# Kernel tuning notes

Measured on AMD Instinct MI355X. Metric: run time of the kernel, lower is better.

The kernel has to match this reference:

```python
import jax, jax.numpy as jnp
import numpy as np

C = 256
NUM_HEADS = 8
GROUPS = 8
EPS = 1e-5


def setup_inputs() -> dict:
    key = jax.random.key(0)
    ks = jax.random.split(key, 7)
    B, H, W = 2, 64, 64
    x = jax.random.normal(ks[0], (B, C, H, W), dtype=jnp.float32)
    gn_weight = jnp.ones((C,), dtype=jnp.float32)
    gn_bias = jnp.zeros((C,), dtype=jnp.float32)
    # 1x1 convs == per-pixel linear layers
    w_qkv = jax.random.normal(ks[1], (3 * C, C), dtype=jnp.float32) * (1.0 / np.sqrt(C))
    b_qkv = jax.random.normal(ks[2], (3 * C,), dtype=jnp.float32) * 0.01
    w_proj = jax.random.normal(ks[3], (C, C), dtype=jnp.float32) * (1.0 / np.sqrt(C))
    b_proj = jax.random.normal(ks[4], (C,), dtype=jnp.float32) * 0.01
    return {"x": x, "gn_weight": gn_weight, "gn_bias": gn_bias,
            "w_qkv": w_qkv, "b_qkv": b_qkv, "w_proj": w_proj, "b_proj": b_proj}


def reference(x, gn_weight, gn_bias, w_qkv, b_qkv, w_proj, b_proj):
    B, Cc, H, W = x.shape
    nh = NUM_HEADS
    hd = Cc // nh
    N = H * W
    scale = hd ** (-0.5)

    # GroupNorm(8, C): normalize over (C/G, H, W) per group, biased variance
    xg = x.reshape(B, GROUPS, Cc // GROUPS, H, W)
    mean = xg.mean(axis=(2, 3, 4), keepdims=True)
    var = xg.var(axis=(2, 3, 4), keepdims=True)
    hn = (xg - mean) * jax.lax.rsqrt(var + EPS)
    hn = hn.reshape(B, Cc, H, W) * gn_weight[None, :, None, None] + gn_bias[None, :, None, None]

    hf = hn.reshape(B, Cc, N)                       # [B, C, N]
    qkv = jnp.einsum('oc,bcn->bon', w_qkv, hf) + b_qkv[None, :, None]  # [B, 3C, N]
    qkv = qkv.reshape(B, 3, nh, hd, N)
    # q,k,v: [B, nh, N, hd]
    q = jnp.transpose(qkv[:, 0], (0, 1, 3, 2))
    k = jnp.transpose(qkv[:, 1], (0, 1, 3, 2))
    v = jnp.transpose(qkv[:, 2], (0, 1, 3, 2))

    attn = jnp.einsum('bhqd,bhkd->bhqk', q, k) * scale  # [B, nh, N, N]
    attn = jax.nn.softmax(attn, axis=-1)
    o = jnp.einsum('bhqk,bhkd->bhqd', attn, v)           # [B, nh, N, hd]
    o = jnp.transpose(o, (0, 1, 3, 2)).reshape(B, Cc, H, W)

    of = o.reshape(B, Cc, N)
    out = jnp.einsum('oc,bcn->bon', w_proj, of) + b_proj[None, :, None]
    return out.reshape(B, Cc, H, W)
```

## Files before the change

### kernel.cpp

```cpp
#include <hip/hip_runtime.h>


typedef _Float16 half8 __attribute__((ext_vector_type(8)));
typedef __fp16   fp16x2 __attribute__((ext_vector_type(2)));
typedef float    f32x4 __attribute__((ext_vector_type(4)));
typedef int      int2v __attribute__((ext_vector_type(2)));
typedef int      int4v __attribute__((ext_vector_type(4)));

__device__ __forceinline__ f32x4 mfma16(half8 a, half8 b, f32x4 c) {
  return __builtin_amdgcn_mfma_f32_16x16x32_f16(a, b, c, 0, 0, 0);
}

#if __has_builtin(__builtin_amdgcn_exp2f)
#define EXP2(x) __builtin_amdgcn_exp2f(x)
#else
#define EXP2(x) exp2f(x)
#endif

__device__ __forceinline__ unsigned short h_bits(_Float16 h) {
  return __builtin_bit_cast(unsigned short, h);
}
__device__ __forceinline__ int h2_bits(fp16x2 h) {
  return __builtin_bit_cast(int, h);
}
__device__ __forceinline__ half8 pack8(f32x4 lo, f32x4 hi) {
  int4v u;
  u[0] = h2_bits(__builtin_amdgcn_cvt_pkrtz(lo[0], lo[1]));
  u[1] = h2_bits(__builtin_amdgcn_cvt_pkrtz(lo[2], lo[3]));
  u[2] = h2_bits(__builtin_amdgcn_cvt_pkrtz(hi[0], hi[1]));
  u[3] = h2_bits(__builtin_amdgcn_cvt_pkrtz(hi[2], hi[3]));
  return __builtin_bit_cast(half8, u);
}

constexpr float CSCALE = (float)(1.4426950408889634 / 5.656854249492381);
constexpr float VSCALE = 0.0009765625f;
constexpr float VUNSC  = 1024.0f;

__global__ __launch_bounds__(256) void gn_stats(const float* __restrict__ x,
                                                float* __restrict__ stats) {
  const int bg = blockIdx.x, ch = blockIdx.y, tid = threadIdx.x;
  const float* p = x + (size_t)bg * 131072 + (size_t)ch * 4096;
  float s = 0.f, ss = 0.f;
#pragma unroll
  for (int j = 0; j < 4; ++j) {
    f32x4 v = *(const f32x4*)(p + j * 1024 + tid * 4);
#pragma unroll
    for (int k = 0; k < 4; ++k) { s += v[k]; ss += v[k] * v[k]; }
  }
#pragma unroll
  for (int m = 1; m <= 32; m <<= 1) { s += __shfl_xor(s, m); ss += __shfl_xor(ss, m); }
  __shared__ float red[8];
  const int wv = tid >> 6;
  if ((tid & 63) == 0) { red[wv * 2] = s; red[wv * 2 + 1] = ss; }
  __syncthreads();
  if (tid == 0) {
    float S = red[0] + red[2] + red[4] + red[6];
    float SS = red[1] + red[3] + red[5] + red[7];
    atomicAdd(&stats[bg * 2], S);
    atomicAdd(&stats[bg * 2 + 1], SS);
  }
}

__global__ __launch_bounds__(256) void gn_apply(const float* __restrict__ x,
                                                const float* __restrict__ gw,
                                                const float* __restrict__ gb,
                                                const float* __restrict__ stats,
                                                _Float16* __restrict__ hn) {
  __shared__ float tile[64 * 65];
  const int tid = threadIdx.x;
  const int a = tid & 15;
  const int row16 = tid >> 4;
  const int b = blockIdx.z, c0 = blockIdx.y * 64, n0 = blockIdx.x * 64;
#pragma unroll
  for (int m = 0; m < 4; ++m) {
    const int cl = row16 + 16 * m;
    const int c = c0 + cl;
    const int g = c >> 5;
    const float s = stats[(b * 8 + g) * 2];
    const float ss = stats[(b * 8 + g) * 2 + 1];
    const float mean = s * (1.f / 131072.f);
    const float var = ss * (1.f / 131072.f) - mean * mean;
    const float rstd = rsqrtf(var + 1e-5f);
    const float ga = gw[c] * rstd;
    const float be = gb[c] - mean * ga;
    f32x4 xv = *(const f32x4*)(x + ((size_t)(b * 256 + c)) * 4096 + n0 + a * 4);
#pragma unroll
    for (int j = 0; j < 4; ++j) tile[cl * 65 + a * 4 + j] = xv[j] * ga + be;
  }
  __syncthreads();
#pragma unroll
  for (int m = 0; m < 4; ++m) {
    const int nl = row16 + 16 * m;
    const int cb = a * 4;
    int2v uh;
    unsigned short hh[4];
#pragma unroll
    for (int j = 0; j < 4; ++j) {
      hh[j] = h_bits((_Float16)tile[(cb + j) * 65 + nl]);
    }
    uh[0] = hh[0] | (hh[1] << 16); uh[1] = hh[2] | (hh[3] << 16);
    size_t off = ((size_t)(b * 4096 + n0 + nl)) * 256 + c0 + cb;
    *(int2v*)(hn + off) = uh;
  }
}

template <int MODE>
__global__ __launch_bounds__(256) void gemm_f16(
    const float* __restrict__ W, const _Float16* __restrict__ Bm,
    const float* __restrict__ bias,
    _Float16* __restrict__ qkT, _Float16* __restrict__ v_t,
    float* __restrict__ outp) {
  __shared__ _Float16 a_lds[2][4096];
  __shared__ _Float16 b_lds[2][4096];
  const int tid = threadIdx.x, lane = tid & 63, wv = tid >> 6;
  const int qq = lane >> 4, ii = lane & 15;
  const int m0 = blockIdx.x * 64, n0 = blockIdx.y * 64, bz = blockIdx.z;

  const float*    asrc[2];
  const _Float16* bsrc[2];
  int dst8[2];
#pragma unroll
  for (int rep = 0; rep < 2; ++rep) {
    const int idx = tid + 256 * rep;
    dst8[rep] = idx * 8;
    const int j = idx >> 7, c = (idx >> 6) & 1, l = idx & 63;
    const int lq = l >> 4, li = l & 15;
    asrc[rep] = W + (size_t)(m0 + 16 * j + li) * 256 + 32 * c + 8 * lq;
    bsrc[rep] = Bm + ((size_t)(bz * 4096 + n0 + 16 * j + li)) * 256 + 32 * c + 8 * lq;
  }

  f32x4 acc[4] = {};

  f32x4 a0a = *(const f32x4*)asrc[0], a0b = *(const f32x4*)(asrc[0] + 4);
  f32x4 a1a = *(const f32x4*)asrc[1], a1b = *(const f32x4*)(asrc[1] + 4);
  half8 br0 = *(const half8*)bsrc[0];
  half8 br1 = *(const half8*)bsrc[1];
  *(half8*)(a_lds[0] + dst8[0]) = pack8(a0a, a0b);
  *(half8*)(a_lds[0] + dst8[1]) = pack8(a1a, a1b);
  *(half8*)(b_lds[0] + dst8[0]) = br0;
  *(half8*)(b_lds[0] + dst8[1]) = br1;
  __syncthreads();

  for (int it = 0; it < 4; ++it) {
    const int cur = it & 1;
    if (it < 3) {
      const int ko = (it + 1) * 64;
      a0a = *(const f32x4*)(asrc[0] + ko);
      a0b = *(const f32x4*)(asrc[0] + ko + 4);
      a1a = *(const f32x4*)(asrc[1] + ko);
      a1b = *(const f32x4*)(asrc[1] + ko + 4);
      br0 = *(const half8*)(bsrc[0] + ko);
      br1 = *(const half8*)(bsrc[1] + ko);
    }
    half8 ah0 = *(const half8*)(a_lds[cur] + ((wv * 2 + 0) * 64 + lane) * 8);
    half8 ah1 = *(const half8*)(a_lds[cur] + ((wv * 2 + 1) * 64 + lane) * 8);
#pragma unroll
    for (int t = 0; t < 4; ++t) {
      half8 b0 = *(const half8*)(b_lds[cur] + ((t * 2 + 0) * 64 + lane) * 8);
      half8 b1 = *(const half8*)(b_lds[cur] + ((t * 2 + 1) * 64 + lane) * 8);
      acc[t] = mfma16(ah0, b0, acc[t]);
      acc[t] = mfma16(ah1, b1, acc[t]);
    }
    if (it < 3) {
      _Float16* an = a_lds[cur ^ 1];
      _Float16* bn = b_lds[cur ^ 1];
      *(half8*)(an + dst8[0]) = pack8(a0a, a0b);
      *(half8*)(an + dst8[1]) = pack8(a1a, a1b);
      *(half8*)(bn + dst8[0]) = br0;
      *(half8*)(bn + dst8[1]) = br1;
    }
    __syncthreads();
  }

  const int och0 = m0 + 16 * wv + 4 * qq;
  if (MODE == 0) {
    if (m0 < 512) {
      const float sc = (m0 < 256) ? CSCALE : 1.0f;
#pragma unroll
      for (int t = 0; t < 4; ++t) {
        const int n = n0 + 16 * t + ii;
        unsigned short hh[4];
#pragma unroll
        for (int r = 0; r < 4; ++r) {
          hh[r] = h_bits((_Float16)((acc[t][r] + bias[och0 + r]) * sc));
        }
        int2v u;
        u[0] = hh[0] | (hh[1] << 16);
        u[1] = hh[2] | (hh[3] << 16);
        *(int2v*)(qkT + ((size_t)(bz * 4096 + n)) * 512 + och0) = u;
      }
    } else {
#pragma unroll
      for (int t = 0; t < 4; ++t) {
#pragma unroll
        for (int r = 0; r < 4; ++r) {
          const int och = och0 + r;
          const int d = och - 512;
          const int hd_ = d & 31, head = d >> 5;
          const int n = n0 + 16 * t + ii;
          v_t[((size_t)((bz * 8 + head) * 32 + hd_)) * 4096 + n] =
              (_Float16)((acc[t][r] + bias[och]) * VSCALE);
        }
      }
    }
  } else {
#pragma unroll
    for (int t = 0; t < 4; ++t) {
#pragma unroll
      for (int r = 0; r < 4; ++r) {
        const int och = och0 + r;
        const int n = n0 + 16 * t + ii;
        outp[((size_t)(bz * 256 + och)) * 4096 + n] = acc[t][r] + bias[och];
      }
    }
  }
}

__global__ __launch_bounds__(256, 8) void attn_kernel(
    const _Float16* __restrict__ qkT, const _Float16* __restrict__ v_t,
    _Float16* __restrict__ opart, float* __restrict__ lpart) {
  __shared__ _Float16 k_lds[2][2048];
  __shared__ _Float16 v_lds[2][2048];
  const int tid = threadIdx.x, lane = tid & 63, wv = tid >> 6;
  const int qq = lane >> 4, ii = lane & 15;
  const int bh = blockIdx.y, b = bh >> 3, h = bh & 7;
  const int n0 = blockIdx.x * 128;
  const int part = blockIdx.z;
  const int key0 = part * 1024;

  const _Float16* qbase =
      qkT + ((size_t)(b * 4096 + n0 + 32 * wv + ii)) * 512 + h * 32 + 8 * qq;
  half8 qf0 = *(const half8*)qbase;
  half8 qf1 = *(const half8*)(qbase + (size_t)16 * 512);

  const int f = tid >> 6, l = tid & 63;
  const int fq = l >> 4, fi = l & 15;
  const int u0 = f >> 1, hf = f & 1;
  const int g = 32 * u0 + 4 * hf + 8 * (fi >> 2) + (fi & 3);
  const _Float16* ksrc =
      qkT + ((size_t)(b * 4096 + key0 + g)) * 512 + 256 + h * 32 + 8 * fq;
  const _Float16* vsrc =
      v_t + ((size_t)(bh * 32 + 16 * hf + fi)) * 4096 + key0 + 32 * u0 + 8 * fq;
  const int dst8 = tid * 8;

  half8 ones8;
#pragma unroll
  for (int j = 0; j < 8; ++j) ones8[j] = (_Float16)1.0f;

  f32x4 o00 = {}, o10 = {}, o01 = {}, o11 = {}, accl0 = {}, accl1 = {};

  half8 kr = *(const half8*)ksrc;
  half8 vr = *(const half8*)vsrc;
  *(half8*)(k_lds[0] + dst8) = kr;
  *(half8*)(v_lds[0] + dst8) = vr;
  __syncthreads();

  for (int kb = 0; kb < 16; ++kb) {
    const int cur = kb & 1;
    if (kb < 15) {
      kr = *(const half8*)(ksrc + (size_t)(kb + 1) * 64 * 512);
      vr = *(const half8*)(vsrc + (size_t)(kb + 1) * 64);
    }
    const _Float16* kbase = k_lds[cur];
    const _Float16* vbase = v_lds[cur];

#pragma unroll
    for (int u = 0; u < 2; ++u) {
      half8 kfa = *(const half8*)(kbase + u * 1024 + lane * 8);
      half8 kfb = *(const half8*)(kbase + u * 1024 + 512 + lane * 8);
      f32x4 z = {};
      f32x4 sa0 = mfma16(kfa, qf0, z);
      f32x4 sb0 = mfma16(kfb, qf0, z);
      f32x4 sa1 = mfma16(kfa, qf1, z);
      f32x4 sb1 = mfma16(kfb, qf1, z);
      int4v p0, p1;
      p0[0] = h2_bits(__builtin_amdgcn_cvt_pkrtz(EXP2(sa0[0]), EXP2(sa0[1])));
      p0[1] = h2_bits(__builtin_amdgcn_cvt_pkrtz(EXP2(sa0[2]), EXP2(sa0[3])));
      p0[2] = h2_bits(__builtin_amdgcn_cvt_pkrtz(EXP2(sb0[0]), EXP2(sb0[1])));
      p0[3] = h2_bits(__builtin_amdgcn_cvt_pkrtz(EXP2(sb0[2]), EXP2(sb0[3])));
      p1[0] = h2_bits(__builtin_amdgcn_cvt_pkrtz(EXP2(sa1[0]), EXP2(sa1[1])));
      p1[1] = h2_bits(__builtin_amdgcn_cvt_pkrtz(EXP2(sa1[2]), EXP2(sa1[3])));
      p1[2] = h2_bits(__builtin_amdgcn_cvt_pkrtz(EXP2(sb1[0]), EXP2(sb1[1])));
      p1[3] = h2_bits(__builtin_amdgcn_cvt_pkrtz(EXP2(sb1[2]), EXP2(sb1[3])));
      half8 pt0 = __builtin_bit_cast(half8, p0);
      half8 pt1 = __builtin_bit_cast(half8, p1);
      half8 vf0 = *(const half8*)(vbase + u * 1024 + lane * 8);
      half8 vf1 = *(const half8*)(vbase + u * 1024 + 512 + lane * 8);
      o00 = mfma16(vf0, pt0, o00);
      o10 = mfma16(vf1, pt0, o10);
      accl0 = mfma16(ones8, pt0, accl0);
      o01 = mfma16(vf0, pt1, o01);
      o11 = mfma16(vf1, pt1, o11);
      accl1 = mfma16(ones8, pt1, accl1);
    }

    if (kb < 15) {
      *(half8*)(k_lds[cur ^ 1] + dst8) = kr;
      *(half8*)(v_lds[cur ^ 1] + dst8) = vr;
    }
    __syncthreads();
  }

#pragma unroll
  for (int hfq = 0; hfq < 2; ++hfq) {
    const f32x4 oa = hfq ? o01 : o00;
    const f32x4 ob = hfq ? o11 : o10;
    const int q = n0 + 32 * wv + 16 * hfq + ii;
    _Float16* base =
        opart + ((size_t)((part * 2 + b) * 4096 + q)) * 256 + h * 32;
    unsigned short hh[4];
#pragma unroll
    for (int r = 0; r < 4; ++r) hh[r] = h_bits((_Float16)oa[r]);
    int2v ua;
    ua[0] = hh[0] | (hh[1] << 16); ua[1] = hh[2] | (hh[3] << 16);
    *(int2v*)(base + 4 * qq) = ua;
#pragma unroll
    for (int r = 0; r < 4; ++r) hh[r] = h_bits((_Float16)ob[r]);
    ua[0] = hh[0] | (hh[1] << 16); ua[1] = hh[2] | (hh[3] << 16);
    *(int2v*)(base + 16 + 4 * qq) = ua;
    if (qq == 0) {
      lpart[((size_t)((part * 2 + b) * 4096 + q)) * 8 + h] =
          hfq ? accl1[0] : accl0[0];
    }
  }
}

__global__ __launch_bounds__(256) void attn_combine(
    const _Float16* __restrict__ opart, const float* __restrict__ lpart,
    _Float16* __restrict__ o16) {
  const int c = threadIdx.x, hh = c >> 5;
#pragma unroll
  for (int k = 0; k < 4; ++k) {
    const int row = blockIdx.x * 4 + k;
    const int b = row >> 12, q = row & 4095;
    float O = 0.f, L = 0.f;
#pragma unroll
    for (int p = 0; p < 4; ++p) {
      O += (float)opart[((size_t)((p * 2 + b) * 4096 + q)) * 256 + c];
      L += lpart[((size_t)((p * 2 + b) * 4096 + q)) * 8 + hh];
    }
    o16[(size_t)row * 256 + c] = (_Float16)(O * (VUNSC / L));
  }
}

extern "C" void kernel_launch(void* const* d_in, const int* in_sizes, int n_in,
                              void* d_out, int out_size, void* d_ws, size_t ws_size,
                              hipStream_t stream) {
  const float* x     = (const float*)d_in[0];
  const float* gnw   = (const float*)d_in[1];
  const float* gnb   = (const float*)d_in[2];
  const float* wqkv  = (const float*)d_in[3];
  const float* bqkv  = (const float*)d_in[4];
  const float* wproj = (const float*)d_in[5];
  const float* bproj = (const float*)d_in[6];
  float* out = (float*)d_out;

  char* ws = (char*)d_ws;
  size_t off = 0;
  auto alloc = [&](size_t bytes) -> char* {
    char* p = ws + off;
    off += (bytes + 255) & ~(size_t)255;
    return p;
  };
  float*    stats  = (float*)alloc(128);
  _Float16* hn     = (_Float16*)alloc((size_t)2 * 4096 * 256 * 2);
  _Float16* qkT    = (_Float16*)alloc((size_t)2 * 4096 * 512 * 2);
  _Float16* v_t    = (_Float16*)alloc((size_t)16 * 32 * 4096 * 2);
  _Float16* opart  = (_Float16*)alloc((size_t)8 * 4096 * 256 * 2);
  float*    lpart  = (float*)alloc((size_t)8 * 4096 * 8 * 4);
  _Float16* o16 = hn;
  if (off > ws_size) return;

  (void)hipMemsetAsync(stats, 0, 256, stream);
  gn_stats<<<dim3(16, 32), 256, 0, stream>>>(x, stats);
  gn_apply<<<dim3(64, 4, 2), 256, 0, stream>>>(x, gnw, gnb, stats, hn);
  gemm_f16<0><<<dim3(12, 64, 2), 256, 0, stream>>>(wqkv, hn, bqkv, qkT, v_t,
                                                   nullptr);
  attn_kernel<<<dim3(32, 16, 4), 256, 0, stream>>>(qkT, v_t, opart, lpart);
  attn_combine<<<2048, 256, 0, stream>>>(opart, lpart, o16);
  gemm_f16<1><<<dim3(4, 64, 2), 256, 0, stream>>>(wproj, o16, bproj, nullptr,
                                                  nullptr, out);
}
```

Measured before the change: 166.1 us.

## Enlarge attention query tile, split keys into 8 parts, pre-cast weights to fp16

The attention kernel now gives each wave 64 queries instead of 32 and splits the keys into 8 parts of 512. Each K/V tile loaded into LDS is therefore reused across four query fragments, which cuts shared-memory loads per MFMA. In exchange the split-K partial buffers double in size and the combine kernel reads eight partials per row, adding memory traffic. Separately, a new kernel casts the QKV and projection weights to fp16 once per call, so the GEMMs load half-size A tiles and skip the in-loop pack conversions, at the cost of one extra launch.

```diff
diff --git a/kernel.cpp b/kernel.cpp
--- a/kernel.cpp
+++ b/kernel.cpp
@@ -22,14 +22,6 @@
 }
 __device__ __forceinline__ int h2_bits(fp16x2 h) {
   return __builtin_bit_cast(int, h);
-}
-__device__ __forceinline__ half8 pack8(f32x4 lo, f32x4 hi) {
-  int4v u;
-  u[0] = h2_bits(__builtin_amdgcn_cvt_pkrtz(lo[0], lo[1]));
-  u[1] = h2_bits(__builtin_amdgcn_cvt_pkrtz(lo[2], lo[3]));
-  u[2] = h2_bits(__builtin_amdgcn_cvt_pkrtz(hi[0], hi[1]));
-  u[3] = h2_bits(__builtin_amdgcn_cvt_pkrtz(hi[2], hi[3]));
-  return __builtin_bit_cast(half8, u);
 }
 
 constexpr float CSCALE = (float)(1.4426950408889634 / 5.656854249492381);
@@ -104,9 +96,21 @@
   }
 }
 
+__global__ __launch_bounds__(256) void wcast(const float* __restrict__ wq,
+                                             const float* __restrict__ wp,
+                                             _Float16* __restrict__ wqh,
+                                             _Float16* __restrict__ wph) {
+  const int idx = blockIdx.x * 256 + threadIdx.x;
+  if (idx < 196608) {
+    wqh[idx] = (_Float16)wq[idx];
+  } else {
+    wph[idx - 196608] = (_Float16)wp[idx - 196608];
+  }
+}
+
 template <int MODE>
 __global__ __launch_bounds__(256) void gemm_f16(
-    const float* __restrict__ W, const _Float16* __restrict__ Bm,
+    const _Float16* __restrict__ W, const _Float16* __restrict__ Bm,
     const float* __restrict__ bias,
     _Float16* __restrict__ qkT, _Float16* __restrict__ v_t,
     float* __restrict__ outp) {
@@ -116,7 +120,7 @@
   const int qq = lane >> 4, ii = lane & 15;
   const int m0 = blockIdx.x * 64, n0 = blockIdx.y * 64, bz = blockIdx.z;
 
-  const float*    asrc[2];
+  const _Float16* asrc[2];
   const _Float16* bsrc[2];
   int dst8[2];
 #pragma unroll
@@ -131,12 +135,12 @@
 
   f32x4 acc[4] = {};
 
-  f32x4 a0a = *(const f32x4*)asrc[0], a0b = *(const f32x4*)(asrc[0] + 4);
-  f32x4 a1a = *(const f32x4*)asrc[1], a1b = *(const f32x4*)(asrc[1] + 4);
+  half8 ar0 = *(const half8*)asrc[0];
+  half8 ar1 = *(const half8*)asrc[1];
   half8 br0 = *(const half8*)bsrc[0];
   half8 br1 = *(const half8*)bsrc[1];
-  *(half8*)(a_lds[0] + dst8[0]) = pack8(a0a, a0b);
-  *(half8*)(a_lds[0] + dst8[1]) = pack8(a1a, a1b);
+  *(half8*)(a_lds[0] + dst8[0]) = ar0;
+  *(half8*)(a_lds[0] + dst8[1]) = ar1;
   *(half8*)(b_lds[0] + dst8[0]) = br0;
   *(half8*)(b_lds[0] + dst8[1]) = br1;
   __syncthreads();
@@ -145,10 +149,8 @@
     const int cur = it & 1;
     if (it < 3) {
       const int ko = (it + 1) * 64;
-      a0a = *(const f32x4*)(asrc[0] + ko);
-      a0b = *(const f32x4*)(asrc[0] + ko + 4);
-      a1a = *(const f32x4*)(asrc[1] + ko);
-      a1b = *(const f32x4*)(asrc[1] + ko + 4);
+      ar0 = *(const half8*)(asrc[0] + ko);
+      ar1 = *(const half8*)(asrc[1] + ko);
       br0 = *(const half8*)(bsrc[0] + ko);
       br1 = *(const half8*)(bsrc[1] + ko);
     }
@@ -164,8 +166,8 @@
     if (it < 3) {
       _Float16* an = a_lds[cur ^ 1];
       _Float16* bn = b_lds[cur ^ 1];
-      *(half8*)(an + dst8[0]) = pack8(a0a, a0b);
-      *(half8*)(an + dst8[1]) = pack8(a1a, a1b);
+      *(half8*)(an + dst8[0]) = ar0;
+      *(half8*)(an + dst8[1]) = ar1;
       *(half8*)(bn + dst8[0]) = br0;
       *(half8*)(bn + dst8[1]) = br1;
     }
@@ -216,7 +218,7 @@
   }
 }
 
-__global__ __launch_bounds__(256, 8) void attn_kernel(
+__global__ __launch_bounds__(256) void attn_kernel(
     const _Float16* __restrict__ qkT, const _Float16* __restrict__ v_t,
     _Float16* __restrict__ opart, float* __restrict__ lpart) {
   __shared__ _Float16 k_lds[2][2048];
@@ -224,14 +226,16 @@
   const int tid = threadIdx.x, lane = tid & 63, wv = tid >> 6;
   const int qq = lane >> 4, ii = lane & 15;
   const int bh = blockIdx.y, b = bh >> 3, h = bh & 7;
-  const int n0 = blockIdx.x * 128;
+  const int n0 = blockIdx.x * 256;
   const int part = blockIdx.z;
-  const int key0 = part * 1024;
+  const int key0 = part * 512;
 
   const _Float16* qbase =
-      qkT + ((size_t)(b * 4096 + n0 + 32 * wv + ii)) * 512 + h * 32 + 8 * qq;
-  half8 qf0 = *(const half8*)qbase;
-  half8 qf1 = *(const half8*)(qbase + (size_t)16 * 512);
+      qkT + ((size_t)(b * 4096 + n0 + 64 * wv + ii)) * 512 + h * 32 + 8 * qq;
+  half8 qf[4];
+#pragma unroll
+  for (int hq = 0; hq < 4; ++hq)
+    qf[hq] = *(const half8*)(qbase + (size_t)(16 * hq) * 512);
 
   const int f = tid >> 6, l = tid & 63;
   const int fq = l >> 4, fi = l & 15;
@@ -247,7 +251,8 @@
 #pragma unroll
   for (int j = 0; j < 8; ++j) ones8[j] = (_Float16)1.0f;
 
-  f32x4 o00 = {}, o10 = {}, o01 = {}, o11 = {}, accl0 = {}, accl1 = {};
+  f32x4 oacc[4][2] = {};
+  f32x4 accl[4] = {};
 
   half8 kr = *(const half8*)ksrc;
   half8 vr = *(const half8*)vsrc;
@@ -255,9 +260,9 @@
   *(half8*)(v_lds[0] + dst8) = vr;
   __syncthreads();
 
-  for (int kb = 0; kb < 16; ++kb) {
+  for (int kb = 0; kb < 8; ++kb) {
     const int cur = kb & 1;
-    if (kb < 15) {
+    if (kb < 7) {
       kr = *(const half8*)(ksrc + (size_t)(kb + 1) * 64 * 512);
       vr = *(const half8*)(vsrc + (size_t)(kb + 1) * 64);
     }
@@ -268,33 +273,26 @@
     for (int u = 0; u < 2; ++u) {
       half8 kfa = *(const half8*)(kbase + u * 1024 + lane * 8);
       half8 kfb = *(const half8*)(kbase + u * 1024 + 512 + lane * 8);
-      f32x4 z = {};
-      f32x4 sa0 = mfma16(kfa, qf0, z);
-      f32x4 sb0 = mfma16(kfb, qf0, z);
-      f32x4 sa1 = mfma16(kfa, qf1, z);
-      f32x4 sb1 = mfma16(kfb, qf1, z);
-      int4v p0, p1;
-      p0[0] = h2_bits(__builtin_amdgcn_cvt_pkrtz(EXP2(sa0[0]), EXP2(sa0[1])));
-      p0[1] = h2_bits(__builtin_amdgcn_cvt_pkrtz(EXP2(sa0[2]), EXP2(sa0[3])));
-      p0[2] = h2_bits(__builtin_amdgcn_cvt_pkrtz(EXP2(sb0[0]), EXP2(sb0[1])));
-      p0[3] = h2_bits(__builtin_amdgcn_cvt_pkrtz(EXP2(sb0[2]), EXP2(sb0[3])));
-      p1[0] = h2_bits(__builtin_amdgcn_cvt_pkrtz(EXP2(sa1[0]), EXP2(sa1[1])));
-      p1[1] = h2_bits(__builtin_amdgcn_cvt_pkrtz(EXP2(sa1[2]), EXP2(sa1[3])));
-      p1[2] = h2_bits(__builtin_amdgcn_cvt_pkrtz(EXP2(sb1[0]), EXP2(sb1[1])));
-      p1[3] = h2_bits(__builtin_amdgcn_cvt_pkrtz(EXP2(sb1[2]), EXP2(sb1[3])));
-      half8 pt0 = __builtin_bit_cast(half8, p0);
-      half8 pt1 = __builtin_bit_cast(half8, p1);
       half8 vf0 = *(const half8*)(vbase + u * 1024 + lane * 8);
       half8 vf1 = *(const half8*)(vbase + u * 1024 + 512 + lane * 8);
-      o00 = mfma16(vf0, pt0, o00);
-      o10 = mfma16(vf1, pt0, o10);
-      accl0 = mfma16(ones8, pt0, accl0);
-      o01 = mfma16(vf0, pt1, o01);
-      o11 = mfma16(vf1, pt1, o11);
-      accl1 = mfma16(ones8, pt1, accl1);
-    }
-
-    if (kb < 15) {
+#pragma unroll
+      for (int hq = 0; hq < 4; ++hq) {
+        f32x4 z = {};
+        f32x4 sa = mfma16(kfa, qf[hq], z);
+        f32x4 sb = mfma16(kfb, qf[hq], z);
+        int4v p;
+        p[0] = h2_bits(__builtin_amdgcn_cvt_pkrtz(EXP2(sa[0]), EXP2(sa[1])));
+        p[1] = h2_bits(__builtin_amdgcn_cvt_pkrtz(EXP2(sa[2]), EXP2(sa[3])));
+        p[2] = h2_bits(__builtin_amdgcn_cvt_pkrtz(EXP2(sb[0]), EXP2(sb[1])));
+        p[3] = h2_bits(__builtin_amdgcn_cvt_pkrtz(EXP2(sb[2]), EXP2(sb[3])));
+        half8 pt = __builtin_bit_cast(half8, p);
+        oacc[hq][0] = mfma16(vf0, pt, oacc[hq][0]);
+        oacc[hq][1] = mfma16(vf1, pt, oacc[hq][1]);
+        accl[hq] = mfma16(ones8, pt, accl[hq]);
+      }
+    }
+
+    if (kb < 7) {
       *(half8*)(k_lds[cur ^ 1] + dst8) = kr;
       *(half8*)(v_lds[cur ^ 1] + dst8) = vr;
     }
@@ -302,25 +300,22 @@
   }
 
 #pragma unroll
-  for (int hfq = 0; hfq < 2; ++hfq) {
-    const f32x4 oa = hfq ? o01 : o00;
-    const f32x4 ob = hfq ? o11 : o10;
-    const int q = n0 + 32 * wv + 16 * hfq + ii;
+  for (int hq = 0; hq < 4; ++hq) {
+    const int q = n0 + 64 * wv + 16 * hq + ii;
     _Float16* base =
         opart + ((size_t)((part * 2 + b) * 4096 + q)) * 256 + h * 32;
     unsigned short hh[4];
-#pragma unroll
-    for (int r = 0; r < 4; ++r) hh[r] = h_bits((_Float16)oa[r]);
     int2v ua;
+#pragma unroll
+    for (int r = 0; r < 4; ++r) hh[r] = h_bits((_Float16)oacc[hq][0][r]);
     ua[0] = hh[0] | (hh[1] << 16); ua[1] = hh[2] | (hh[3] << 16);
     *(int2v*)(base + 4 * qq) = ua;
 #pragma unroll
-    for (int r = 0; r < 4; ++r) hh[r] = h_bits((_Float16)ob[r]);
+    for (int r = 0; r < 4; ++r) hh[r] = h_bits((_Float16)oacc[hq][1][r]);
     ua[0] = hh[0] | (hh[1] << 16); ua[1] = hh[2] | (hh[3] << 16);
     *(int2v*)(base + 16 + 4 * qq) = ua;
     if (qq == 0) {
-      lpart[((size_t)((part * 2 + b) * 4096 + q)) * 8 + h] =
-          hfq ? accl1[0] : accl0[0];
+      lpart[((size_t)((part * 2 + b) * 4096 + q)) * 8 + h] = accl[hq][0];
     }
   }
 }
@@ -335,7 +330,7 @@
     const int b = row >> 12, q = row & 4095;
     float O = 0.f, L = 0.f;
 #pragma unroll
-    for (int p = 0; p < 4; ++p) {
+    for (int p = 0; p < 8; ++p) {
       O += (float)opart[((size_t)((p * 2 + b) * 4096 + q)) * 256 + c];
       L += lpart[((size_t)((p * 2 + b) * 4096 + q)) * 8 + hh];
     }
@@ -364,20 +359,23 @@
   };
   float*    stats  = (float*)alloc(128);
   _Float16* hn     = (_Float16*)alloc((size_t)2 * 4096 * 256 * 2);
+  _Float16* wq_h   = (_Float16*)alloc((size_t)768 * 256 * 2);
+  _Float16* wp_h   = (_Float16*)alloc((size_t)256 * 256 * 2);
   _Float16* qkT    = (_Float16*)alloc((size_t)2 * 4096 * 512 * 2);
   _Float16* v_t    = (_Float16*)alloc((size_t)16 * 32 * 4096 * 2);
-  _Float16* opart  = (_Float16*)alloc((size_t)8 * 4096 * 256 * 2);
-  float*    lpart  = (float*)alloc((size_t)8 * 4096 * 8 * 4);
+  _Float16* opart  = (_Float16*)alloc((size_t)16 * 4096 * 256 * 2);
+  float*    lpart  = (float*)alloc((size_t)16 * 4096 * 8 * 4);
   _Float16* o16 = hn;
   if (off > ws_size) return;
 
   (void)hipMemsetAsync(stats, 0, 256, stream);
   gn_stats<<<dim3(16, 32), 256, 0, stream>>>(x, stats);
   gn_apply<<<dim3(64, 4, 2), 256, 0, stream>>>(x, gnw, gnb, stats, hn);
-  gemm_f16<0><<<dim3(12, 64, 2), 256, 0, stream>>>(wqkv, hn, bqkv, qkT, v_t,
+  wcast<<<1024, 256, 0, stream>>>(wqkv, wproj, wq_h, wp_h);
+  gemm_f16<0><<<dim3(12, 64, 2), 256, 0, stream>>>(wq_h, hn, bqkv, qkT, v_t,
                                                    nullptr);
-  attn_kernel<<<dim3(32, 16, 4), 256, 0, stream>>>(qkT, v_t, opart, lpart);
+  attn_kernel<<<dim3(16, 16, 8), 256, 0, stream>>>(qkT, v_t, opart, lpart);
   attn_combine<<<2048, 256, 0, stream>>>(opart, lpart, o16);
-  gemm_f16<1><<<dim3(4, 64, 2), 256, 0, stream>>>(wproj, o16, bproj, nullptr,
+  gemm_f16<1><<<dim3(4, 64, 2), 256, 0, stream>>>(wp_h, o16, bproj, nullptr,
                                                   nullptr, out);
 }
```

Result: no change. 164.7 us (-0.9%).

## Pre-convert weights to fp16 and split attention keys into eight partitions

Applied to the files above, without the earlier changes.

The GN stats kernel now also converts the QKV and projection weights to fp16 in extra blocks, so the GEMMs load half-precision weights directly instead of converting fp32 on every tile. Attention key splitting goes from 4 to 8 partitions of 512 keys each, run as two launches of 4 partitions. The combine kernel then sums 8 partials. This trades larger partial buffers and more combine traffic plus an extra launch for shorter per-block loops.

```diff
diff --git a/kernel.cpp b/kernel.cpp
--- a/kernel.cpp
+++ b/kernel.cpp
@@ -23,41 +23,47 @@
 __device__ __forceinline__ int h2_bits(fp16x2 h) {
   return __builtin_bit_cast(int, h);
 }
-__device__ __forceinline__ half8 pack8(f32x4 lo, f32x4 hi) {
-  int4v u;
-  u[0] = h2_bits(__builtin_amdgcn_cvt_pkrtz(lo[0], lo[1]));
-  u[1] = h2_bits(__builtin_amdgcn_cvt_pkrtz(lo[2], lo[3]));
-  u[2] = h2_bits(__builtin_amdgcn_cvt_pkrtz(hi[0], hi[1]));
-  u[3] = h2_bits(__builtin_amdgcn_cvt_pkrtz(hi[2], hi[3]));
-  return __builtin_bit_cast(half8, u);
-}
 
 constexpr float CSCALE = (float)(1.4426950408889634 / 5.656854249492381);
 constexpr float VSCALE = 0.0009765625f;
 constexpr float VUNSC  = 1024.0f;
 
-__global__ __launch_bounds__(256) void gn_stats(const float* __restrict__ x,
-                                                float* __restrict__ stats) {
-  const int bg = blockIdx.x, ch = blockIdx.y, tid = threadIdx.x;
-  const float* p = x + (size_t)bg * 131072 + (size_t)ch * 4096;
-  float s = 0.f, ss = 0.f;
-#pragma unroll
-  for (int j = 0; j < 4; ++j) {
-    f32x4 v = *(const f32x4*)(p + j * 1024 + tid * 4);
-#pragma unroll
-    for (int k = 0; k < 4; ++k) { s += v[k]; ss += v[k] * v[k]; }
-  }
-#pragma unroll
-  for (int m = 1; m <= 32; m <<= 1) { s += __shfl_xor(s, m); ss += __shfl_xor(ss, m); }
-  __shared__ float red[8];
-  const int wv = tid >> 6;
-  if ((tid & 63) == 0) { red[wv * 2] = s; red[wv * 2 + 1] = ss; }
-  __syncthreads();
-  if (tid == 0) {
-    float S = red[0] + red[2] + red[4] + red[6];
-    float SS = red[1] + red[3] + red[5] + red[7];
-    atomicAdd(&stats[bg * 2], S);
-    atomicAdd(&stats[bg * 2 + 1], SS);
+__global__ __launch_bounds__(256) void prep(const float* __restrict__ x,
+                                            float* __restrict__ stats,
+                                            const float* __restrict__ wq,
+                                            const float* __restrict__ wp,
+                                            _Float16* __restrict__ wqh,
+                                            _Float16* __restrict__ wph) {
+  const int tid = threadIdx.x;
+  if (blockIdx.x < 512) {
+    const int bg = blockIdx.x >> 5, ch = blockIdx.x & 31;
+    const float* p = x + (size_t)bg * 131072 + (size_t)ch * 4096;
+    float s = 0.f, ss = 0.f;
+#pragma unroll
+    for (int j = 0; j < 4; ++j) {
+      f32x4 v = *(const f32x4*)(p + j * 1024 + tid * 4);
+#pragma unroll
+      for (int k = 0; k < 4; ++k) { s += v[k]; ss += v[k] * v[k]; }
+    }
+#pragma unroll
+    for (int m = 1; m <= 32; m <<= 1) { s += __shfl_xor(s, m); ss += __shfl_xor(ss, m); }
+    __shared__ float red[8];
+    const int wv = tid >> 6;
+    if ((tid & 63) == 0) { red[wv * 2] = s; red[wv * 2 + 1] = ss; }
+    __syncthreads();
+    if (tid == 0) {
+      float S = red[0] + red[2] + red[4] + red[6];
+      float SS = red[1] + red[3] + red[5] + red[7];
+      atomicAdd(&stats[bg * 2], S);
+      atomicAdd(&stats[bg * 2 + 1], SS);
+    }
+  } else {
+    const int idx = (blockIdx.x - 512) * 256 + tid;
+    if (idx < 196608) {
+      wqh[idx] = (_Float16)wq[idx];
+    } else {
+      wph[idx - 196608] = (_Float16)wp[idx - 196608];
+    }
   }
 }
 
@@ -106,7 +112,7 @@
 
 template <int MODE>
 __global__ __launch_bounds__(256) void gemm_f16(
-    const float* __restrict__ W, const _Float16* __restrict__ Bm,
+    const _Float16* __restrict__ W, const _Float16* __restrict__ Bm,
     const float* __restrict__ bias,
     _Float16* __restrict__ qkT, _Float16* __restrict__ v_t,
     float* __restrict__ outp) {
@@ -116,7 +122,7 @@
   const int qq = lane >> 4, ii = lane & 15;
   const int m0 = blockIdx.x * 64, n0 = blockIdx.y * 64, bz = blockIdx.z;
 
-  const float*    asrc[2];
+  const _Float16* asrc[2];
   const _Float16* bsrc[2];
   int dst8[2];
 #pragma unroll
@@ -131,12 +137,12 @@
 
   f32x4 acc[4] = {};
 
-  f32x4 a0a = *(const f32x4*)asrc[0], a0b = *(const f32x4*)(asrc[0] + 4);
-  f32x4 a1a = *(const f32x4*)asrc[1], a1b = *(const f32x4*)(asrc[1] + 4);
+  half8 ar0 = *(const half8*)asrc[0];
+  half8 ar1 = *(const half8*)asrc[1];
   half8 br0 = *(const half8*)bsrc[0];
   half8 br1 = *(const half8*)bsrc[1];
-  *(half8*)(a_lds[0] + dst8[0]) = pack8(a0a, a0b);
-  *(half8*)(a_lds[0] + dst8[1]) = pack8(a1a, a1b);
+  *(half8*)(a_lds[0] + dst8[0]) = ar0;
+  *(half8*)(a_lds[0] + dst8[1]) = ar1;
   *(half8*)(b_lds[0] + dst8[0]) = br0;
   *(half8*)(b_lds[0] + dst8[1]) = br1;
   __syncthreads();
@@ -145,10 +151,8 @@
     const int cur = it & 1;
     if (it < 3) {
       const int ko = (it + 1) * 64;
-      a0a = *(const f32x4*)(asrc[0] + ko);
-      a0b = *(const f32x4*)(asrc[0] + ko + 4);
-      a1a = *(const f32x4*)(asrc[1] + ko);
-      a1b = *(const f32x4*)(asrc[1] + ko + 4);
+      ar0 = *(const half8*)(asrc[0] + ko);
+      ar1 = *(const half8*)(asrc[1] + ko);
       br0 = *(const half8*)(bsrc[0] + ko);
       br1 = *(const half8*)(bsrc[1] + ko);
     }
@@ -164,8 +168,8 @@
     if (it < 3) {
       _Float16* an = a_lds[cur ^ 1];
       _Float16* bn = b_lds[cur ^ 1];
-      *(half8*)(an + dst8[0]) = pack8(a0a, a0b);
-      *(half8*)(an + dst8[1]) = pack8(a1a, a1b);
+      *(half8*)(an + dst8[0]) = ar0;
+      *(half8*)(an + dst8[1]) = ar1;
       *(half8*)(bn + dst8[0]) = br0;
       *(half8*)(bn + dst8[1]) = br1;
     }
@@ -218,15 +222,15 @@
 
 __global__ __launch_bounds__(256, 8) void attn_kernel(
     const _Float16* __restrict__ qkT, const _Float16* __restrict__ v_t,
-    _Float16* __restrict__ opart, float* __restrict__ lpart) {
+    _Float16* __restrict__ opart, float* __restrict__ lpart, int pbase) {
   __shared__ _Float16 k_lds[2][2048];
   __shared__ _Float16 v_lds[2][2048];
   const int tid = threadIdx.x, lane = tid & 63, wv = tid >> 6;
   const int qq = lane >> 4, ii = lane & 15;
   const int bh = blockIdx.y, b = bh >> 3, h = bh & 7;
   const int n0 = blockIdx.x * 128;
-  const int part = blockIdx.z;
-  const int key0 = part * 1024;
+  const int part = pbase + blockIdx.z;
+  const int key0 = part * 512;
 
   const _Float16* qbase =
       qkT + ((size_t)(b * 4096 + n0 + 32 * wv + ii)) * 512 + h * 32 + 8 * qq;
@@ -255,9 +259,9 @@
   *(half8*)(v_lds[0] + dst8) = vr;
   __syncthreads();
 
-  for (int kb = 0; kb < 16; ++kb) {
+  for (int kb = 0; kb < 8; ++kb) {
     const int cur = kb & 1;
-    if (kb < 15) {
+    if (kb < 7) {
       kr = *(const half8*)(ksrc + (size_t)(kb + 1) * 64 * 512);
       vr = *(const half8*)(vsrc + (size_t)(kb + 1) * 64);
     }
@@ -294,7 +298,7 @@
       accl1 = mfma16(ones8, pt1, accl1);
     }
 
-    if (kb < 15) {
+    if (kb < 7) {
       *(half8*)(k_lds[cur ^ 1] + dst8) = kr;
       *(half8*)(v_lds[cur ^ 1] + dst8) = vr;
     }
@@ -309,9 +313,9 @@
     _Float16* base =
         opart + ((size_t)((part * 2 + b) * 4096 + q)) * 256 + h * 32;
     unsigned short hh[4];
+    int2v ua;
 #pragma unroll
     for (int r = 0; r < 4; ++r) hh[r] = h_bits((_Float16)oa[r]);
-    int2v ua;
     ua[0] = hh[0] | (hh[1] << 16); ua[1] = hh[2] | (hh[3] << 16);
     *(int2v*)(base + 4 * qq) = ua;
 #pragma unroll
@@ -335,7 +339,7 @@
     const int b = row >> 12, q = row & 4095;
     float O = 0.f, L = 0.f;
 #pragma unroll
-    for (int p = 0; p < 4; ++p) {
+    for (int p = 0; p < 8; ++p) {
       O += (float)opart[((size_t)((p * 2 + b) * 4096 + q)) * 256 + c];
       L += lpart[((size_t)((p * 2 + b) * 4096 + q)) * 8 + hh];
     }
@@ -364,20 +368,23 @@
   };
   float*    stats  = (float*)alloc(128);
   _Float16* hn     = (_Float16*)alloc((size_t)2 * 4096 * 256 * 2);
+  _Float16* wq_h   = (_Float16*)alloc((size_t)768 * 256 * 2);
+  _Float16* wp_h   = (_Float16*)alloc((size_t)256 * 256 * 2);
   _Float16* qkT    = (_Float16*)alloc((size_t)2 * 4096 * 512 * 2);
   _Float16* v_t    = (_Float16*)alloc((size_t)16 * 32 * 4096 * 2);
-  _Float16* opart  = (_Float16*)alloc((size_t)8 * 4096 * 256 * 2);
-  float*    lpart  = (float*)alloc((size_t)8 * 4096 * 8 * 4);
+  _Float16* opart  = (_Float16*)alloc((size_t)16 * 4096 * 256 * 2);
+  float*    lpart  = (float*)alloc((size_t)16 * 4096 * 8 * 4);
   _Float16* o16 = hn;
   if (off > ws_size) return;
 
   (void)hipMemsetAsync(stats, 0, 256, stream);
-  gn_stats<<<dim3(16, 32), 256, 0, stream>>>(x, stats);
+  prep<<<1536, 256, 0, stream>>>(x, stats, wqkv, wproj, wq_h, wp_h);
   gn_apply<<<dim3(64, 4, 2), 256, 0, stream>>>(x, gnw, gnb, stats, hn);
-  gemm_f16<0><<<dim3(12, 64, 2), 256, 0, stream>>>(wqkv, hn, bqkv, qkT, v_t,
+  gemm_f16<0><<<dim3(12, 64, 2), 256, 0, stream>>>(wq_h, hn, bqkv, qkT, v_t,
                                                    nullptr);
-  attn_kernel<<<dim3(32, 16, 4), 256, 0, stream>>>(qkT, v_t, opart, lpart);
+  attn_kernel<<<dim3(32, 16, 4), 256, 0, stream>>>(qkT, v_t, opart, lpart, 0);
+  attn_kernel<<<dim3(32, 16, 4), 256, 0, stream>>>(qkT, v_t, opart, lpart, 4);
   attn_combine<<<2048, 256, 0, stream>>>(opart, lpart, o16);
-  gemm_f16<1><<<dim3(4, 64, 2), 256, 0, stream>>>(wproj, o16, bproj, nullptr,
+  gemm_f16<1><<<dim3(4, 64, 2), 256, 0, stream>>>(wp_h, o16, bproj, nullptr,
                                                   nullptr, out);
 }
```

Result: slower. 185.6 us (+11.7%).
